# Kernel optimization log

Hardware: AMD Instinct MI355X
Metric: run time of the kernel (lower is better)

Reference implementation:

```python
import jax, jax.numpy as jnp
import numpy as np


def setup_inputs() -> dict:
    key = jax.random.key(0)
    k1, k2 = jax.random.split(key)
    x = jax.random.normal(k1, (2, 256, 512, 512), dtype=jnp.float32)
    # torch.rand -> uniform [0, 1)
    kernel = jax.random.uniform(k2, (1, 256, 11, 11), dtype=jnp.float32)
    bias = jnp.zeros((1,), dtype=jnp.float32)
    return {"x": x, "kernel": kernel, "bias": bias}


def reference(x, kernel, bias):
    # Faithful to the original: output[:, 0, i, j] = sum over BATCH, channels,
    # and kernel window of (patch * kernel), i.e. the reduction includes the
    # batch dim, and the same scalar map is broadcast to every batch element.
    # sum_b(patch_b) == patch(sum_b x), so this collapses to one VALID conv
    # over the batch-summed input.
    B = x.shape[0]
    xs = jnp.sum(x, axis=0, keepdims=True)  # [1, C, H, W]
    out = jax.lax.conv_general_dilated(
        xs, kernel,
        window_strides=(1, 1),
        padding='VALID',
        dimension_numbers=('NCHW', 'OIHW', 'NCHW'),
    )  # [1, 1, O, O]
    out = jnp.broadcast_to(out, (B,) + out.shape[1:])  # [B, 1, O, O]
    return out + bias  # bias (1,) broadcasts over all dims
```

## Files before the change

kernel.cpp:

```cpp
#include <hip/hip_runtime.h>

#define H   512
#define W   512
#define C   256
#define KH  11
#define KW  11
#define OH  502
#define OW  502
#define OUT_MAP (OH * OW)
#define HWSZ (H * W)

#define TX 4
#define TY 4
#define TILE_X 64
#define TILE_Y 64
#define IN_X  (TILE_X + KW - 1)
#define IN_Y  (TILE_Y + KH - 1)
#define IN_XP 76
#define CPB   16
#define VEC_PER_ROW 19
#define NSTAGE_TOT (IN_Y * VEC_PER_ROW)
#define NSTAGE_IT  6

__global__ __launch_bounds__(256, 4)
void conv_kernel(const float* __restrict__ x, const float* __restrict__ w,
                 float* __restrict__ out)
{
    __shared__ float s_in[IN_Y * IN_XP];

    const int tid = threadIdx.x;
    const int tx  = tid & 15;
    const int ty  = tid >> 4;
    const int x0  = blockIdx.x * TILE_X;
    const int y0  = blockIdx.y * TILE_Y;
    const int c0  = blockIdx.z * CPB;

    int s_goff[NSTAGE_IT];
    int s_loff[NSTAGE_IT];
    bool s_act[NSTAGE_IT];
#pragma unroll
    for (int j = 0; j < NSTAGE_IT; ++j) {
        int i = tid + j * 256;
        const bool act = (i < NSTAGE_TOT);
        if (!act) i = 0;
        const int row = i / VEC_PER_ROW;
        const int vec = i - row * VEC_PER_ROW;
        const int gy  = min(y0 + row, H - 1);
        const int gx  = min(x0 + vec * 4, W - 4);
        s_goff[j] = gy * W + gx;
        s_loff[j] = row * IN_XP + vec * 4;
        s_act[j]  = act;
    }

    float acc[TY][TX];
#pragma unroll
    for (int dy = 0; dy < TY; ++dy)
#pragma unroll
        for (int i = 0; i < TX; ++i) acc[dy][i] = 0.f;

    const int ry0 = ty * TY;
    const int cx0 = tx * TX;

    float4 pa[NSTAGE_IT], pb[NSTAGE_IT];
    {
        const float* __restrict__ p0 = x + (size_t)c0 * HWSZ;
        const float* __restrict__ p1 = p0 + (size_t)C * HWSZ;
#pragma unroll
        for (int j = 0; j < NSTAGE_IT; ++j) {
            pa[j] = *(const float4*)(p0 + s_goff[j]);
            pb[j] = *(const float4*)(p1 + s_goff[j]);
        }
    }

#pragma unroll 1
    for (int cc = 0; cc < CPB; ++cc) {
#pragma unroll
        for (int j = 0; j < NSTAGE_IT; ++j) {
            if (s_act[j]) {
                *(float4*)&s_in[s_loff[j]] =
                    make_float4(pa[j].x + pb[j].x, pa[j].y + pb[j].y,
                                pa[j].z + pb[j].z, pa[j].w + pb[j].w);
            }
        }
        __syncthreads();

        if (cc + 1 < CPB) {
            const float* __restrict__ p0 = x + (size_t)(c0 + cc + 1) * HWSZ;
            const float* __restrict__ p1 = p0 + (size_t)C * HWSZ;
#pragma unroll
            for (int j = 0; j < NSTAGE_IT; ++j) {
                pa[j] = *(const float4*)(p0 + s_goff[j]);
                pb[j] = *(const float4*)(p1 + s_goff[j]);
            }
        }

        const float* __restrict__ wc = w + (size_t)(c0 + cc) * (KH * KW);
#pragma unroll
        for (int r = 0; r < TY + KH - 1; ++r) {
            const float* rp = &s_in[(ry0 + r) * IN_XP + cx0];
            const float4 a0 = *(const float4*)(rp + 0);
            const float4 a1 = *(const float4*)(rp + 4);
            const float4 a2 = *(const float4*)(rp + 8);
            const float4 a3 = *(const float4*)(rp + 12);
            const float win[16] = {a0.x, a0.y, a0.z, a0.w,
                                   a1.x, a1.y, a1.z, a1.w,
                                   a2.x, a2.y, a2.z, a2.w,
                                   a3.x, a3.y, a3.z, a3.w};
#pragma unroll
            for (int dy = 0; dy < TY; ++dy) {
                const int kh = r - dy;
                if (kh >= 0 && kh < KH) {
#pragma unroll
                    for (int kw = 0; kw < KW; ++kw) {
                        const float wv = wc[kh * KW + kw];
#pragma unroll
                        for (int i = 0; i < TX; ++i)
                            acc[dy][i] += win[kw + i] * wv;
                    }
                }
            }
        }
        __syncthreads();
    }

#pragma unroll
    for (int dy = 0; dy < TY; ++dy) {
        const int oy = y0 + ry0 + dy;
        if (oy < OH) {
#pragma unroll
            for (int i = 0; i < TX; ++i) {
                const int ox = x0 + cx0 + i;
                if (ox < OW)
                    atomicAdd(&out[(size_t)oy * OW + ox], acc[dy][i]);
            }
        }
    }
}

__global__ void init_kernel(float* __restrict__ out, const float* __restrict__ bias)
{
    const int i = blockIdx.x * 256 + threadIdx.x;
    if (i < OUT_MAP) out[i] = bias[0];
}

__global__ void bcast_kernel(float* __restrict__ out)
{
    const int i = blockIdx.x * 256 + threadIdx.x;
    if (i < OUT_MAP) out[OUT_MAP + i] = out[i];
}

extern "C" void kernel_launch(void* const* d_in, const int* in_sizes, int n_in,
                              void* d_out, int out_size, void* d_ws, size_t ws_size,
                              hipStream_t stream)
{
    const float* x    = (const float*)d_in[0];
    const float* w    = (const float*)d_in[1];
    const float* bias = (const float*)d_in[2];
    float* out = (float*)d_out;

    const int nb = (OUT_MAP + 255) / 256;
    init_kernel<<<nb, 256, 0, stream>>>(out, bias);
    conv_kernel<<<dim3(8, 8, 16), 256, 0, stream>>>(x, w, out);
    bcast_kernel<<<nb, 256, 0, stream>>>(out);
}
```

Before: 816.7 us.

## Retile conv to 8x2 outputs per thread with LDS weights and swizzled input

```diff
diff --git a/kernel.cpp b/kernel.cpp
--- a/kernel.cpp
+++ b/kernel.cpp
@@ -10,23 +10,31 @@
 #define OUT_MAP (OH * OW)
 #define HWSZ (H * W)
 
-#define TX 4
-#define TY 4
-#define TILE_X 64
-#define TILE_Y 64
-#define IN_X  (TILE_X + KW - 1)
+#define TX 8
+#define TY 2
+#define TILE_X 128
+#define TILE_Y 32
 #define IN_Y  (TILE_Y + KH - 1)
-#define IN_XP 76
+#define UPR   35
+#define IN_XP (UPR * 4)
 #define CPB   16
-#define VEC_PER_ROW 19
-#define NSTAGE_TOT (IN_Y * VEC_PER_ROW)
+#define NSTAGE_TOT (IN_Y * UPR)
 #define NSTAGE_IT  6
+#define WPC 132
+
+__device__ __forceinline__ int swz(int u) { return u ^ ((u >> 3) & 1); }
+
+#define AV(j)   ((j & 3) == 0 ? av[(j) >> 2].x : (j & 3) == 1 ? av[(j) >> 2].y : \
+                 (j & 3) == 2 ? av[(j) >> 2].z : av[(j) >> 2].w)
+#define WVS(q, j) ((j & 3) == 0 ? q[(j) >> 2].x : (j & 3) == 1 ? q[(j) >> 2].y : \
+                   (j & 3) == 2 ? q[(j) >> 2].z : q[(j) >> 2].w)
 
 __global__ __launch_bounds__(256, 4)
 void conv_kernel(const float* __restrict__ x, const float* __restrict__ w,
                  float* __restrict__ out)
 {
     __shared__ float s_in[IN_Y * IN_XP];
+    __shared__ float s_w[CPB * WPC];
 
     const int tid = threadIdx.x;
     const int tx  = tid & 15;
@@ -35,21 +43,25 @@
     const int y0  = blockIdx.y * TILE_Y;
     const int c0  = blockIdx.z * CPB;
 
-    int s_goff[NSTAGE_IT];
-    int s_loff[NSTAGE_IT];
-    bool s_act[NSTAGE_IT];
+    for (int it = tid; it < CPB * 121; it += 256) {
+        const int ch  = it / 121;
+        const int rem = it - ch * 121;
+        const int kh  = rem / 11;
+        const int kw  = rem - kh * 11;
+        s_w[ch * WPC + kh * 12 + kw] = w[(size_t)(c0 + ch) * 121 + rem];
+    }
+
+    int s_goff[NSTAGE_IT], s_loff[NSTAGE_IT];
 #pragma unroll
     for (int j = 0; j < NSTAGE_IT; ++j) {
         int i = tid + j * 256;
-        const bool act = (i < NSTAGE_TOT);
-        if (!act) i = 0;
-        const int row = i / VEC_PER_ROW;
-        const int vec = i - row * VEC_PER_ROW;
+        if (i >= NSTAGE_TOT) i = NSTAGE_TOT - 1;
+        const int row = i / UPR;
+        const int vec = i - row * UPR;
         const int gy  = min(y0 + row, H - 1);
         const int gx  = min(x0 + vec * 4, W - 4);
         s_goff[j] = gy * W + gx;
-        s_loff[j] = row * IN_XP + vec * 4;
-        s_act[j]  = act;
+        s_loff[j] = row * IN_XP + swz(vec) * 4;
     }
 
     float acc[TY][TX];
@@ -58,8 +70,11 @@
 #pragma unroll
         for (int i = 0; i < TX; ++i) acc[dy][i] = 0.f;
 
-    const int ry0 = ty * TY;
-    const int cx0 = tx * TX;
+    const int ry0  = ty * TY;
+    const int cx0u = tx * 2;
+    int roff[5];
+#pragma unroll
+    for (int k = 0; k < 5; ++k) roff[k] = swz(cx0u + k) * 4;
 
     float4 pa[NSTAGE_IT], pb[NSTAGE_IT];
     {
@@ -75,13 +90,10 @@
 #pragma unroll 1
     for (int cc = 0; cc < CPB; ++cc) {
 #pragma unroll
-        for (int j = 0; j < NSTAGE_IT; ++j) {
-            if (s_act[j]) {
-                *(float4*)&s_in[s_loff[j]] =
-                    make_float4(pa[j].x + pb[j].x, pa[j].y + pb[j].y,
-                                pa[j].z + pb[j].z, pa[j].w + pb[j].w);
-            }
-        }
+        for (int j = 0; j < NSTAGE_IT; ++j)
+            *(float4*)&s_in[s_loff[j]] =
+                make_float4(pa[j].x + pb[j].x, pa[j].y + pb[j].y,
+                            pa[j].z + pb[j].z, pa[j].w + pb[j].w);
         __syncthreads();
 
         if (cc + 1 < CPB) {
@@ -94,29 +106,39 @@
             }
         }
 
-        const float* __restrict__ wc = w + (size_t)(c0 + cc) * (KH * KW);
+        const float* __restrict__ swc = s_w + cc * WPC;
+        float4 wr[2][3];
 #pragma unroll
         for (int r = 0; r < TY + KH - 1; ++r) {
-            const float* rp = &s_in[(ry0 + r) * IN_XP + cx0];
-            const float4 a0 = *(const float4*)(rp + 0);
-            const float4 a1 = *(const float4*)(rp + 4);
-            const float4 a2 = *(const float4*)(rp + 8);
-            const float4 a3 = *(const float4*)(rp + 12);
-            const float win[16] = {a0.x, a0.y, a0.z, a0.w,
-                                   a1.x, a1.y, a1.z, a1.w,
-                                   a2.x, a2.y, a2.z, a2.w,
-                                   a3.x, a3.y, a3.z, a3.w};
+            const float* rp = &s_in[(ry0 + r) * IN_XP];
+            float4 av[5];
 #pragma unroll
-            for (int dy = 0; dy < TY; ++dy) {
-                const int kh = r - dy;
-                if (kh >= 0 && kh < KH) {
+            for (int k = 0; k < 5; ++k)
+                av[k] = *(const float4*)(rp + roff[k]);
+
+            if (r < KH) {
+                const float* wrow = swc + r * 12;
+                wr[r & 1][0] = *(const float4*)(wrow + 0);
+                wr[r & 1][1] = *(const float4*)(wrow + 4);
+                wr[r & 1][2] = *(const float4*)(wrow + 8);
+            }
+
+            if (r < KH) {
 #pragma unroll
-                    for (int kw = 0; kw < KW; ++kw) {
-                        const float wv = wc[kh * KW + kw];
+                for (int kw = 0; kw < KW; ++kw) {
+                    const float wv = WVS(wr[r & 1], kw);
 #pragma unroll
-                        for (int i = 0; i < TX; ++i)
-                            acc[dy][i] += win[kw + i] * wv;
-                    }
+                    for (int i = 0; i < TX; ++i)
+                        acc[0][i] += AV(kw + i) * wv;
+                }
+            }
+            if (r >= 1) {
+#pragma unroll
+                for (int kw = 0; kw < KW; ++kw) {
+                    const float wv = WVS(wr[(r - 1) & 1], kw);
+#pragma unroll
+                    for (int i = 0; i < TX; ++i)
+                        acc[1][i] += AV(kw + i) * wv;
                 }
             }
         }
@@ -129,7 +151,7 @@
         if (oy < OH) {
 #pragma unroll
             for (int i = 0; i < TX; ++i) {
-                const int ox = x0 + cx0 + i;
+                const int ox = x0 + tx * TX + i;
                 if (ox < OW)
                     atomicAdd(&out[(size_t)oy * OW + ox], acc[dy][i]);
             }
@@ -160,6 +182,6 @@
 
     const int nb = (OUT_MAP + 255) / 256;
     init_kernel<<<nb, 256, 0, stream>>>(out, bias);
-    conv_kernel<<<dim3(8, 8, 16), 256, 0, stream>>>(x, w, out);
+    conv_kernel<<<dim3(4, 16, 16), 256, 0, stream>>>(x, w, out);
     bcast_kernel<<<nb, 256, 0, stream>>>(out);
 }
```

Measured after the change: 899.3 us. +10.1%, slower.

## Double-buffer input slab, stage weights in LDS, and software-pipeline row loads

Applied to the files above, without the earlier changes.

```diff
diff --git a/kernel.cpp b/kernel.cpp
--- a/kernel.cpp
+++ b/kernel.cpp
@@ -14,19 +14,60 @@
 #define TY 4
 #define TILE_X 64
 #define TILE_Y 64
-#define IN_X  (TILE_X + KW - 1)
 #define IN_Y  (TILE_Y + KH - 1)
 #define IN_XP 76
-#define CPB   16
+#define SLAB  (IN_Y * IN_XP)
 #define VEC_PER_ROW 19
 #define NSTAGE_TOT (IN_Y * VEC_PER_ROW)
 #define NSTAGE_IT  6
-
-__global__ __launch_bounds__(256, 4)
+#define CPB   32
+#define WROW  12
+#define WPC   (KH * WROW)
+
+#define AVAL(A, j) ((j & 3) == 0 ? A[(j) >> 2].x : (j & 3) == 1 ? A[(j) >> 2].y : \
+                    (j & 3) == 2 ? A[(j) >> 2].z : A[(j) >> 2].w)
+#define WVAL(s, j) ((j & 3) == 0 ? wr[s][(j) >> 2].x : (j & 3) == 1 ? wr[s][(j) >> 2].y : \
+                    (j & 3) == 2 ? wr[s][(j) >> 2].z : wr[s][(j) >> 2].w)
+
+#define ROW(r, AVC, AVN)                                                      \
+  {                                                                           \
+    if ((r) < TY + KH - 2) {                                                  \
+      _Pragma("unroll")                                                       \
+      for (int k = 0; k < 4; ++k)                                             \
+        AVN[k] = *(const float4*)(rbase + ((r) + 1) * IN_XP + k * 4);         \
+    }                                                                         \
+    if ((r) - 3 >= 0 && (r) - 3 < KH) {     \
+      _Pragma("unroll")                                                       \
+      for (int kw = 0; kw < KW; ++kw) {                                       \
+        const float wv = WVAL(((r) - 3) & 3, kw);                             \
+        _Pragma("unroll")                                                     \
+        for (int i = 0; i < TX; ++i) acc[3][i] += AVAL(AVC, kw + i) * wv;     \
+      }                                                                       \
+    }                                                                         \
+    if ((r) + 1 < KH) {                   \
+      wr[((r) + 1) & 3][0] = *(const float4*)(swc + ((r) + 1) * WROW + 0);    \
+      wr[((r) + 1) & 3][1] = *(const float4*)(swc + ((r) + 1) * WROW + 4);    \
+      wr[((r) + 1) & 3][2] = *(const float4*)(swc + ((r) + 1) * WROW + 8);    \
+    }                                                                         \
+    _Pragma("unroll")                                                         \
+    for (int dy = 0; dy < 3; ++dy) {                                          \
+      if ((r) - dy >= 0 && (r) - dy < KH) {                                   \
+        _Pragma("unroll")                                                     \
+        for (int kw = 0; kw < KW; ++kw) {                                     \
+          const float wv = WVAL(((r) - dy) & 3, kw);                          \
+          _Pragma("unroll")                                                   \
+          for (int i = 0; i < TX; ++i) acc[dy][i] += AVAL(AVC, kw + i) * wv;  \
+        }                                                                     \
+      }                                                                       \
+    }                                                                         \
+  }
+
+__global__ __launch_bounds__(256, 2)
 void conv_kernel(const float* __restrict__ x, const float* __restrict__ w,
                  float* __restrict__ out)
 {
-    __shared__ float s_in[IN_Y * IN_XP];
+    __shared__ float s_in[2][SLAB];
+    __shared__ float s_w[CPB * WPC];
 
     const int tid = threadIdx.x;
     const int tx  = tid & 15;
@@ -35,21 +76,25 @@
     const int y0  = blockIdx.y * TILE_Y;
     const int c0  = blockIdx.z * CPB;
 
-    int s_goff[NSTAGE_IT];
-    int s_loff[NSTAGE_IT];
-    bool s_act[NSTAGE_IT];
+    for (int it = tid; it < CPB * (KH * KW); it += 256) {
+        const int ch  = it / 121;
+        const int rem = it - ch * 121;
+        const int kh  = rem / 11;
+        const int kw  = rem - kh * 11;
+        s_w[ch * WPC + kh * WROW + kw] = w[(size_t)(c0 + ch) * 121 + rem];
+    }
+
+    int s_goff[NSTAGE_IT], s_loff[NSTAGE_IT];
 #pragma unroll
     for (int j = 0; j < NSTAGE_IT; ++j) {
         int i = tid + j * 256;
-        const bool act = (i < NSTAGE_TOT);
-        if (!act) i = 0;
+        if (i >= NSTAGE_TOT) i = NSTAGE_TOT - 1;
         const int row = i / VEC_PER_ROW;
         const int vec = i - row * VEC_PER_ROW;
         const int gy  = min(y0 + row, H - 1);
         const int gx  = min(x0 + vec * 4, W - 4);
         s_goff[j] = gy * W + gx;
         s_loff[j] = row * IN_XP + vec * 4;
-        s_act[j]  = act;
     }
 
     float acc[TY][TX];
@@ -70,20 +115,18 @@
             pa[j] = *(const float4*)(p0 + s_goff[j]);
             pb[j] = *(const float4*)(p1 + s_goff[j]);
         }
-    }
-
+        float* dbase = s_in[0];
+#pragma unroll
+        for (int j = 0; j < NSTAGE_IT; ++j)
+            *(float4*)(dbase + s_loff[j]) =
+                make_float4(pa[j].x + pb[j].x, pa[j].y + pb[j].y,
+                            pa[j].z + pb[j].z, pa[j].w + pb[j].w);
+    }
+    __syncthreads();
+
+    int cur = 0;
 #pragma unroll 1
     for (int cc = 0; cc < CPB; ++cc) {
-#pragma unroll
-        for (int j = 0; j < NSTAGE_IT; ++j) {
-            if (s_act[j]) {
-                *(float4*)&s_in[s_loff[j]] =
-                    make_float4(pa[j].x + pb[j].x, pa[j].y + pb[j].y,
-                                pa[j].z + pb[j].z, pa[j].w + pb[j].w);
-            }
-        }
-        __syncthreads();
-
         if (cc + 1 < CPB) {
             const float* __restrict__ p0 = x + (size_t)(c0 + cc + 1) * HWSZ;
             const float* __restrict__ p1 = p0 + (size_t)C * HWSZ;
@@ -94,33 +137,31 @@
             }
         }
 
-        const float* __restrict__ wc = w + (size_t)(c0 + cc) * (KH * KW);
-#pragma unroll
-        for (int r = 0; r < TY + KH - 1; ++r) {
-            const float* rp = &s_in[(ry0 + r) * IN_XP + cx0];
-            const float4 a0 = *(const float4*)(rp + 0);
-            const float4 a1 = *(const float4*)(rp + 4);
-            const float4 a2 = *(const float4*)(rp + 8);
-            const float4 a3 = *(const float4*)(rp + 12);
-            const float win[16] = {a0.x, a0.y, a0.z, a0.w,
-                                   a1.x, a1.y, a1.z, a1.w,
-                                   a2.x, a2.y, a2.z, a2.w,
-                                   a3.x, a3.y, a3.z, a3.w};
-#pragma unroll
-            for (int dy = 0; dy < TY; ++dy) {
-                const int kh = r - dy;
-                if (kh >= 0 && kh < KH) {
-#pragma unroll
-                    for (int kw = 0; kw < KW; ++kw) {
-                        const float wv = wc[kh * KW + kw];
-#pragma unroll
-                        for (int i = 0; i < TX; ++i)
-                            acc[dy][i] += win[kw + i] * wv;
-                    }
-                }
-            }
-        }
-        __syncthreads();
+        const float* rbase = s_in[cur] + ry0 * IN_XP + cx0;
+        const float* swc   = s_w + cc * WPC;
+        float4 wr[4][3];
+        float4 av0[4], av1[4];
+#pragma unroll
+        for (int k = 0; k < 4; ++k) av0[k] = *(const float4*)(rbase + k * 4);
+        wr[0][0] = *(const float4*)(swc + 0);
+        wr[0][1] = *(const float4*)(swc + 4);
+        wr[0][2] = *(const float4*)(swc + 8);
+
+        ROW(0,  av0, av1); ROW(1,  av1, av0); ROW(2,  av0, av1); ROW(3,  av1, av0);
+        ROW(4,  av0, av1); ROW(5,  av1, av0); ROW(6,  av0, av1); ROW(7,  av1, av0);
+        ROW(8,  av0, av1); ROW(9,  av1, av0); ROW(10, av0, av1); ROW(11, av1, av0);
+        ROW(12, av0, av1); ROW(13, av1, av0);
+
+        if (cc + 1 < CPB) {
+            float* dbase = s_in[cur ^ 1];
+#pragma unroll
+            for (int j = 0; j < NSTAGE_IT; ++j)
+                *(float4*)(dbase + s_loff[j]) =
+                    make_float4(pa[j].x + pb[j].x, pa[j].y + pb[j].y,
+                                pa[j].z + pb[j].z, pa[j].w + pb[j].w);
+            __syncthreads();
+        }
+        cur ^= 1;
     }
 
 #pragma unroll
@@ -160,6 +201,6 @@
 
     const int nb = (OUT_MAP + 255) / 256;
     init_kernel<<<nb, 256, 0, stream>>>(out, bias);
-    conv_kernel<<<dim3(8, 8, 16), 256, 0, stream>>>(x, w, out);
+    conv_kernel<<<dim3(8, 8, 8), 256, 0, stream>>>(x, w, out);
     bcast_kernel<<<nb, 256, 0, stream>>>(out);
 }
```

New measurement: 1.901 ms. 2.33x slower.

## Stage input tiles with async global-to-LDS loads and triple-buffered slabs

Applied to the files above, without the earlier changes.

```diff
diff --git a/kernel.cpp b/kernel.cpp
--- a/kernel.cpp
+++ b/kernel.cpp
@@ -14,19 +14,26 @@
 #define TY 4
 #define TILE_X 64
 #define TILE_Y 64
-#define IN_X  (TILE_X + KW - 1)
-#define IN_Y  (TILE_Y + KH - 1)
+#define IN_Y  74
+#define UPR   19
 #define IN_XP 76
+#define NSTAGE_TOT (IN_Y * UPR)
+#define NSTAGE_IT  6
+#define SLABF (NSTAGE_TOT * 4)
 #define CPB   16
-#define VEC_PER_ROW 19
-#define NSTAGE_TOT (IN_Y * VEC_PER_ROW)
-#define NSTAGE_IT  6
 
-__global__ __launch_bounds__(256, 4)
+__device__ __forceinline__ void gload16(const float* g, float* l)
+{
+    __builtin_amdgcn_global_load_lds(
+        (const __attribute__((address_space(1))) void*)g,
+        (__attribute__((address_space(3))) void*)l, 16, 0, 0);
+}
+
+__global__ __launch_bounds__(256, 2)
 void conv_kernel(const float* __restrict__ x, const float* __restrict__ w,
                  float* __restrict__ out)
 {
-    __shared__ float s_in[IN_Y * IN_XP];
+    __shared__ float s_slab[3][SLABF];
 
     const int tid = threadIdx.x;
     const int tx  = tid & 15;
@@ -35,22 +42,21 @@
     const int y0  = blockIdx.y * TILE_Y;
     const int c0  = blockIdx.z * CPB;
 
-    int s_goff[NSTAGE_IT];
-    int s_loff[NSTAGE_IT];
+    int  s_goff[NSTAGE_IT];
     bool s_act[NSTAGE_IT];
 #pragma unroll
     for (int j = 0; j < NSTAGE_IT; ++j) {
         int i = tid + j * 256;
         const bool act = (i < NSTAGE_TOT);
         if (!act) i = 0;
-        const int row = i / VEC_PER_ROW;
-        const int vec = i - row * VEC_PER_ROW;
+        const int row = i / UPR;
+        const int vec = i - row * UPR;
         const int gy  = min(y0 + row, H - 1);
         const int gx  = min(x0 + vec * 4, W - 4);
         s_goff[j] = gy * W + gx;
-        s_loff[j] = row * IN_XP + vec * 4;
         s_act[j]  = act;
     }
+    const int wub = (tid >> 6) * 64;
 
     float acc[TY][TX];
 #pragma unroll
@@ -61,43 +67,54 @@
     const int ry0 = ty * TY;
     const int cx0 = tx * TX;
 
-    float4 pa[NSTAGE_IT], pb[NSTAGE_IT];
     {
-        const float* __restrict__ p0 = x + (size_t)c0 * HWSZ;
-        const float* __restrict__ p1 = p0 + (size_t)C * HWSZ;
+        const float* p0 = x + (size_t)c0 * HWSZ;
+        const float* p1 = p0 + (size_t)C * HWSZ;
 #pragma unroll
         for (int j = 0; j < NSTAGE_IT; ++j) {
-            pa[j] = *(const float4*)(p0 + s_goff[j]);
-            pb[j] = *(const float4*)(p1 + s_goff[j]);
+            if (s_act[j]) {
+                gload16(p0 + s_goff[j], &s_slab[0][(j * 256 + wub) * 4]);
+                gload16(p1 + s_goff[j], &s_slab[1][(j * 256 + wub) * 4]);
+            }
         }
     }
 
+    float* sa = s_slab[0];
+    float* sb = s_slab[1];
+    float* sf = s_slab[2];
+
 #pragma unroll 1
     for (int cc = 0; cc < CPB; ++cc) {
+        __syncthreads();
+
 #pragma unroll
         for (int j = 0; j < NSTAGE_IT; ++j) {
             if (s_act[j]) {
-                *(float4*)&s_in[s_loff[j]] =
-                    make_float4(pa[j].x + pb[j].x, pa[j].y + pb[j].y,
-                                pa[j].z + pb[j].z, pa[j].w + pb[j].w);
+                const int o = (tid + j * 256) * 4;
+                const float4 a = *(const float4*)&sa[o];
+                const float4 b = *(const float4*)&sb[o];
+                *(float4*)&sa[o] =
+                    make_float4(a.x + b.x, a.y + b.y, a.z + b.z, a.w + b.w);
             }
         }
         __syncthreads();
 
         if (cc + 1 < CPB) {
-            const float* __restrict__ p0 = x + (size_t)(c0 + cc + 1) * HWSZ;
-            const float* __restrict__ p1 = p0 + (size_t)C * HWSZ;
+            const float* p0 = x + (size_t)(c0 + cc + 1) * HWSZ;
+            const float* p1 = p0 + (size_t)C * HWSZ;
 #pragma unroll
             for (int j = 0; j < NSTAGE_IT; ++j) {
-                pa[j] = *(const float4*)(p0 + s_goff[j]);
-                pb[j] = *(const float4*)(p1 + s_goff[j]);
+                if (s_act[j]) {
+                    gload16(p0 + s_goff[j], &sb[(j * 256 + wub) * 4]);
+                    gload16(p1 + s_goff[j], &sf[(j * 256 + wub) * 4]);
+                }
             }
         }
 
         const float* __restrict__ wc = w + (size_t)(c0 + cc) * (KH * KW);
 #pragma unroll
         for (int r = 0; r < TY + KH - 1; ++r) {
-            const float* rp = &s_in[(ry0 + r) * IN_XP + cx0];
+            const float* rp = &sa[(ry0 + r) * IN_XP + cx0];
             const float4 a0 = *(const float4*)(rp + 0);
             const float4 a1 = *(const float4*)(rp + 4);
             const float4 a2 = *(const float4*)(rp + 8);
@@ -120,7 +137,8 @@
                 }
             }
         }
-        __syncthreads();
+
+        float* t = sa; sa = sb; sb = sf; sf = t;
     }
 
 #pragma unroll
```

Measured after the change: 866.3 us. 6.1% more time.
